# Optimization experiments

Hardware: AMD Instinct MI355X
Metric: run time of the kernel (lower is better)

## Reference

```python
import jax, jax.numpy as jnp
from jax import lax
import numpy as np

N = 400000   # active voxels
C = 32       # channels (in == out -> identity downsample)
G = 192      # voxel grid side
K = 27       # 3x3x3 kernel offsets
EPS = 1e-6


def _build_neighbor_map():
    """Rulebook for a 3^3 sparse conv: nbr[k, i] = input index of the voxel at
    coords[i] + offset[k], or -1 if that site is inactive."""
    rng = np.random.default_rng(0)
    keys = rng.choice(G ** 3, size=N, replace=False).astype(np.int64)
    xs = keys // (G * G)
    ys = (keys // G) % G
    zs = keys % G
    order = np.argsort(keys)
    sk = keys[order]
    nbr = np.full((K, N), -1, dtype=np.int32)
    k = 0
    for dx in (-1, 0, 1):
        for dy in (-1, 0, 1):
            for dz in (-1, 0, 1):
                nx, ny, nz = xs + dx, ys + dy, zs + dz
                inb = (nx >= 0) & (nx < G) & (ny >= 0) & (ny < G) & (nz >= 0) & (nz < G)
                nkey = nx * (G * G) + ny * G + nz
                pos = np.clip(np.searchsorted(sk, nkey), 0, N - 1)
                found = inb & (sk[pos] == nkey)
                nbr[k] = np.where(found, order[pos].astype(np.int32), -1)
                k += 1
    return nbr


def setup_inputs() -> dict:
    key = jax.random.key(0)
    k1, k2, k3 = jax.random.split(key, 3)
    scale = 1.0 / np.sqrt(K * C)
    x = jax.random.normal(k1, (N, C), dtype=jnp.float32)
    W1 = jax.random.normal(k2, (K, C, C), dtype=jnp.float32) * scale
    W2 = jax.random.normal(k3, (K, C, C), dtype=jnp.float32) * scale
    return {
        "x": x,
        "nbr": jnp.asarray(_build_neighbor_map()),
        "W1": W1,
        "g1": jnp.ones((C,), jnp.float32),
        "b1": jnp.zeros((C,), jnp.float32),
        "W2": W2,
        "g2": jnp.ones((C,), jnp.float32),
        "b2": jnp.zeros((C,), jnp.float32),
    }


def _sparse_conv(feats, W, nbr):
    # gather-GEMM-scatter over the 27 kernel offsets (stride=1: out sites == in sites)
    def body(acc, kw):
        idx, Wk = kw
        m = idx >= 0
        g = jnp.where(m[:, None], feats[jnp.maximum(idx, 0)], 0.0)  # [N, Cin]
        return acc + g @ Wk, None

    acc = jnp.zeros((feats.shape[0], W.shape[-1]), feats.dtype)
    acc, _ = lax.scan(body, acc, (nbr, W))
    return acc


def _layernorm(h, g, b):
    mu = jnp.mean(h, axis=-1, keepdims=True)
    var = jnp.mean(jnp.square(h - mu), axis=-1, keepdims=True)
    return (h - mu) * lax.rsqrt(var + EPS) * g + b


def reference(x, nbr, W1, g1, b1, W2, g2, b2):
    h = jax.nn.relu(_layernorm(_sparse_conv(x, W1, nbr), g1, b1))
    h = _layernorm(_sparse_conv(h, W2, nbr), g2, b2)
    # downsample is identity (in_channels == out_channels, stride == 1)
    return jax.nn.relu(h + x)
```

## Files before the change

### kernel.cpp

```cpp
#include <hip/hip_runtime.h>
#include <hip/hip_bf16.h>


#define NV 400000

typedef __bf16 bf16x8 __attribute__((ext_vector_type(8)));
typedef float  f32x4  __attribute__((ext_vector_type(4)));

union ABu { bf16x8 v; int4 i4; unsigned short us[8]; };

__device__ __forceinline__ unsigned short rb_f2bf(float f) {
    unsigned int u = __float_as_uint(f);
    return (unsigned short)((u + 0x7fffu + ((u >> 16) & 1u)) >> 16);
}

#define KIDX(kk) ((kk) + ((kk) >= 13 ? 1 : 0))

#define MFMA_BF16 __builtin_amdgcn_mfma_f32_16x16x32_bf16

__global__ __launch_bounds__(512) void xcvt_kernel(const float* __restrict__ xf,
                                                   unsigned short* __restrict__ xb)
{
    size_t i = ((size_t)blockIdx.x * 512 + threadIdx.x) * 8;
    float4 p0 = *(const float4*)(xf + i);
    float4 p1 = *(const float4*)(xf + i + 4);
    ABu a;
    a.us[0] = rb_f2bf(p0.x); a.us[1] = rb_f2bf(p0.y);
    a.us[2] = rb_f2bf(p0.z); a.us[3] = rb_f2bf(p0.w);
    a.us[4] = rb_f2bf(p1.x); a.us[5] = rb_f2bf(p1.y);
    a.us[6] = rb_f2bf(p1.z); a.us[7] = rb_f2bf(p1.w);
    *(int4*)(xb + i) = a.i4;
}

#define GATHER4(gbuf, jall)                                                   \
    do {                                                                      \
        _Pragma("unroll")                                                     \
        for (int _t = 0; _t < 4; ++_t) {                                      \
            int _j = __shfl((jall), _t * 16 + n);                             \
            gbuf[_t] = make_int4(0, 0, 0, 0);                                 \
            if (_j >= 0)                                                      \
                gbuf[_t] = *(const int4*)(gsrc + ((size_t)_j << 5) + qo);     \
        }                                                                     \
    } while (0)

#define CONSUME(kk, gbuf)                                                     \
    do {                                                                      \
        ABu _b0, _b1;                                                         \
        _b0.i4 = *(const int4*)(Bp + (kk) * 1024 + lane * 8);                 \
        _b1.i4 = *(const int4*)(Bp + (kk) * 1024 + 512 + lane * 8);           \
        _Pragma("unroll")                                                     \
        for (int _t = 0; _t < 4; ++_t) {                                      \
            ABu _a; _a.i4 = gbuf[_t];                                         \
            acc[_t][0] = MFMA_BF16(_a.v, _b0.v, acc[_t][0], 0, 0, 0);         \
            acc[_t][1] = MFMA_BF16(_a.v, _b1.v, acc[_t][1], 0, 0, 0);         \
        }                                                                     \
    } while (0)

template <bool WRITE_OUT>
__global__ __launch_bounds__(512, 4) void ResidualBlock_37452114821416_kernel(
    const float* __restrict__ xf,
    const int*   __restrict__ nbr,
    const float* __restrict__ Wf,
    const float* __restrict__ gf,
    const float* __restrict__ bfv,
    float*       __restrict__ outf,
    unsigned short* __restrict__ hbuf,
    const unsigned short* __restrict__ gsrc)
{
    __shared__ __align__(16) unsigned short Bp[26 * 1024];
    for (int e = threadIdx.x; e < 26 * 1024; e += 512) {
        int kk = e >> 10;
        int k  = KIDX(kk);
        int r  = e & 1023;
        int f  = r >> 9;
        int ll = (r >> 3) & 63;
        int j  = r & 7;
        int ci = ((ll >> 4) << 3) + j;
        int co = (ll & 15) + (f << 4);
        Bp[e] = rb_f2bf(Wf[k * 1024 + ci * 32 + co]);
    }

    const int  lane = threadIdx.x & 63;
    const int  wv   = threadIdx.x >> 6;
    const int  q    = lane >> 4, n = lane & 15;
    const int  i0   = blockIdx.x * 512 + wv * 64;
    const int  v64  = i0 + lane;
    const bool okv  = v64 < NV;
    const int  qo   = q * 8;

    ABu cb0, cb1;
    #pragma unroll
    for (int j = 0; j < 8; ++j) {
        int ci = (q << 3) + j;
        cb0.us[j] = rb_f2bf(Wf[13 * 1024 + ci * 32 + n]);
        cb1.us[j] = rb_f2bf(Wf[13 * 1024 + ci * 32 + n + 16]);
    }
    __syncthreads();

    f32x4 acc[4][2];
    #pragma unroll
    for (int t = 0; t < 4; ++t) {
        acc[t][0] = (f32x4){0.f, 0.f, 0.f, 0.f};
        acc[t][1] = (f32x4){0.f, 0.f, 0.f, 0.f};
    }

    int jA = okv ? __builtin_nontemporal_load(nbr + (size_t)KIDX(0) * NV + v64) : -1;
    int jB = okv ? __builtin_nontemporal_load(nbr + (size_t)KIDX(1) * NV + v64) : -1;

    int4 cgb[4];
    #pragma unroll
    for (int t = 0; t < 4; ++t) {
        int vt = i0 + t * 16 + n;
        cgb[t] = make_int4(0, 0, 0, 0);
        if (vt < NV) cgb[t] = *(const int4*)(gsrc + ((size_t)vt << 5) + qo);
    }

    int4 gA[4], gB[4];
    GATHER4(gA, jA);
    GATHER4(gB, jB);

    int jE = okv ? __builtin_nontemporal_load(nbr + (size_t)KIDX(2) * NV + v64) : -1;
    int jO = okv ? __builtin_nontemporal_load(nbr + (size_t)KIDX(3) * NV + v64) : -1;

    #pragma unroll
    for (int t = 0; t < 4; ++t) {
        ABu a; a.i4 = cgb[t];
        acc[t][0] = MFMA_BF16(a.v, cb0.v, acc[t][0], 0, 0, 0);
        acc[t][1] = MFMA_BF16(a.v, cb1.v, acc[t][1], 0, 0, 0);
    }

    #pragma unroll
    for (int p = 0; p < 13; ++p) {
        int jE2 = -1, jO2 = -1;
        if (2 * p + 4 < 26 && okv)
            jE2 = __builtin_nontemporal_load(nbr + (size_t)KIDX(2 * p + 4) * NV + v64);
        if (2 * p + 5 < 26 && okv)
            jO2 = __builtin_nontemporal_load(nbr + (size_t)KIDX(2 * p + 5) * NV + v64);

        CONSUME(2 * p, gA);
        if (2 * p + 2 < 26) GATHER4(gA, jE);

        CONSUME(2 * p + 1, gB);
        if (2 * p + 3 < 26) GATHER4(gB, jO);

        jE = jE2; jO = jO2;
    }

    const float gv0 = gf[n],  gv1 = gf[n + 16];
    const float bv0 = bfv[n], bv1 = bfv[n + 16];
    #pragma unroll
    for (int t = 0; t < 4; ++t) {
        #pragma unroll
        for (int r = 0; r < 4; ++r) {
            float x0 = acc[t][0][r], x1 = acc[t][1][r];
            float s  = x0 + x1;
            float ss = x0 * x0 + x1 * x1;
            #pragma unroll
            for (int mm = 1; mm <= 8; mm <<= 1) {
                s  += __shfl_xor(s, mm);
                ss += __shfl_xor(ss, mm);
            }
            float mu  = s * (1.f / 32.f);
            float var = ss * (1.f / 32.f) - mu * mu;
            float rs  = rsqrtf(var + 1e-6f);
            int vv = i0 + t * 16 + q * 4 + r;
            if (vv < NV) {
                float y0 = (x0 - mu) * rs * gv0 + bv0;
                float y1 = (x1 - mu) * rs * gv1 + bv1;
                if constexpr (WRITE_OUT) {
                    y0 += xf[(size_t)vv * 32 + n];
                    y1 += xf[(size_t)vv * 32 + n + 16];
                    outf[(size_t)vv * 32 + n]      = fmaxf(y0, 0.f);
                    outf[(size_t)vv * 32 + n + 16] = fmaxf(y1, 0.f);
                } else {
                    hbuf[(size_t)vv * 32 + n]      = rb_f2bf(fmaxf(y0, 0.f));
                    hbuf[(size_t)vv * 32 + n + 16] = rb_f2bf(fmaxf(y1, 0.f));
                }
            }
        }
    }
}

__global__ __launch_bounds__(512, 4) void pass1_f32_kernel(
    const float* __restrict__ xf, const int* __restrict__ nbr,
    const float* __restrict__ Wf, const float* __restrict__ gf,
    const float* __restrict__ bfv, unsigned short* __restrict__ hbuf)
{
    __shared__ __align__(16) unsigned short Bp[27 * 1024];
    for (int e = threadIdx.x; e < 27 * 1024; e += 512) {
        int k = e >> 10, r = e & 1023, f = r >> 9;
        int ll = (r >> 3) & 63, j = r & 7;
        int ci = ((ll >> 4) << 3) + j, co = (ll & 15) + (f << 4);
        Bp[e] = rb_f2bf(Wf[k * 1024 + ci * 32 + co]);
    }
    __syncthreads();
    const int lane = threadIdx.x & 63, wv = threadIdx.x >> 6;
    const int q = lane >> 4, n = lane & 15;
    const int i0 = blockIdx.x * 512 + wv * 64;
    f32x4 acc[4][2];
    #pragma unroll
    for (int t = 0; t < 4; ++t) { acc[t][0] = (f32x4){0,0,0,0}; acc[t][1] = (f32x4){0,0,0,0}; }
    for (int k = 0; k < 27; ++k) {
        ABu b0, b1;
        b0.i4 = *(const int4*)(Bp + k * 1024 + lane * 8);
        b1.i4 = *(const int4*)(Bp + k * 1024 + 512 + lane * 8);
        const int* nb = nbr + (size_t)k * NV;
        #pragma unroll
        for (int t = 0; t < 4; ++t) {
            int v = i0 + t * 16 + n;
            int jn = (v < NV) ? nb[v] : -1;
            if (__ballot(jn >= 0) == 0ull) continue;
            ABu a; a.i4 = make_int4(0, 0, 0, 0);
            if (jn >= 0) {
                const float* src = xf + (size_t)jn * 32 + q * 8;
                float4 p0 = *(const float4*)(src);
                float4 p1 = *(const float4*)(src + 4);
                a.us[0] = rb_f2bf(p0.x); a.us[1] = rb_f2bf(p0.y);
                a.us[2] = rb_f2bf(p0.z); a.us[3] = rb_f2bf(p0.w);
                a.us[4] = rb_f2bf(p1.x); a.us[5] = rb_f2bf(p1.y);
                a.us[6] = rb_f2bf(p1.z); a.us[7] = rb_f2bf(p1.w);
            }
            acc[t][0] = MFMA_BF16(a.v, b0.v, acc[t][0], 0, 0, 0);
            acc[t][1] = MFMA_BF16(a.v, b1.v, acc[t][1], 0, 0, 0);
        }
    }
    const float gv0 = gf[n], gv1 = gf[n + 16];
    const float bv0 = bfv[n], bv1 = bfv[n + 16];
    #pragma unroll
    for (int t = 0; t < 4; ++t) {
        #pragma unroll
        for (int r = 0; r < 4; ++r) {
            float x0 = acc[t][0][r], x1 = acc[t][1][r];
            float s = x0 + x1, ss = x0 * x0 + x1 * x1;
            #pragma unroll
            for (int mm = 1; mm <= 8; mm <<= 1) { s += __shfl_xor(s, mm); ss += __shfl_xor(ss, mm); }
            float mu = s * (1.f / 32.f);
            float var = ss * (1.f / 32.f) - mu * mu;
            float rs = rsqrtf(var + 1e-6f);
            int vv = i0 + t * 16 + q * 4 + r;
            if (vv < NV) {
                float y0 = (x0 - mu) * rs * gv0 + bv0;
                float y1 = (x1 - mu) * rs * gv1 + bv1;
                hbuf[(size_t)vv * 32 + n]      = rb_f2bf(fmaxf(y0, 0.f));
                hbuf[(size_t)vv * 32 + n + 16] = rb_f2bf(fmaxf(y1, 0.f));
            }
        }
    }
}

extern "C" void kernel_launch(void* const* d_in, const int* in_sizes, int n_in,
                              void* d_out, int out_size, void* d_ws, size_t ws_size,
                              hipStream_t stream)
{
    const float* x   = (const float*)d_in[0];
    const int*   nbr = (const int*)d_in[1];
    const float* W1  = (const float*)d_in[2];
    const float* g1  = (const float*)d_in[3];
    const float* b1  = (const float*)d_in[4];
    const float* W2  = (const float*)d_in[5];
    const float* g2  = (const float*)d_in[6];
    const float* b2  = (const float*)d_in[7];
    float* out = (float*)d_out;

    unsigned short* h  = (unsigned short*)d_ws;
    unsigned short* xb = h + (size_t)NV * 32;
    const bool have_xb = ws_size >= (size_t)NV * 32 * 2 * 2;

    const int nblk = (NV + 511) / 512;

    if (have_xb) {
        xcvt_kernel<<<3125, 512, 0, stream>>>(x, xb);
        ResidualBlock_37452114821416_kernel<false><<<nblk, 512, 0, stream>>>(
            x, nbr, W1, g1, b1, out, h, xb);
    } else {
        pass1_f32_kernel<<<nblk, 512, 0, stream>>>(x, nbr, W1, g1, b1, h);
    }
    ResidualBlock_37452114821416_kernel<true><<<nblk, 512, 0, stream>>>(
        x, nbr, W2, g2, b2, out, h, h);

    (void)in_sizes; (void)n_in; (void)out_size;
}
```

Before: 276.9 us.

## Halve voxels per wave and prefetch neighbor indices seven pairs deep

Each wave now handles 32 voxels instead of 64. Each neighbor-index load fetches two kernel offsets at once, using the two half-waves. Seven index pairs are issued up front, before the weights are staged into shared memory, and kept in a rotating register ring. Gathers are double-buffered by offset pair, and launch bounds are raised to 6 blocks per SM. The aim is to hide gather and index latency with more in-flight loads and more waves, at the cost of twice as many blocks each redoing the shared weight staging, and fewer MFMAs per B-fragment load.

```diff
diff --git a/kernel.cpp b/kernel.cpp
--- a/kernel.cpp
+++ b/kernel.cpp
@@ -32,32 +32,46 @@
     *(int4*)(xb + i) = a.i4;
 }
 
-#define GATHER4(gbuf, jall)                                                   \
+#define LOADIDX(P)                                                            \
+    (okv ? __builtin_nontemporal_load(                                        \
+               nbr + (size_t)KIDX(2 * (P)) * NV +                             \
+               (size_t)((KIDX(2 * (P) + 1) - KIDX(2 * (P))) * NVhi + vIdx))   \
+         : -1)
+
+#define GATHER_PAIR(S, JREG)                                                  \
     do {                                                                      \
         _Pragma("unroll")                                                     \
-        for (int _t = 0; _t < 4; ++_t) {                                      \
-            int _j = __shfl((jall), _t * 16 + n);                             \
-            gbuf[_t] = make_int4(0, 0, 0, 0);                                 \
-            if (_j >= 0)                                                      \
-                gbuf[_t] = *(const int4*)(gsrc + ((size_t)_j << 5) + qo);     \
+        for (int _h = 0; _h < 2; ++_h) {                                      \
+            _Pragma("unroll")                                                 \
+            for (int _t = 0; _t < 2; ++_t) {                                  \
+                int _j = __shfl((JREG), _h * 32 + _t * 16 + n);               \
+                g##S[_h][_t] = make_int4(0, 0, 0, 0);                         \
+                if (_j >= 0)                                                  \
+                    g##S[_h][_t] =                                            \
+                        *(const int4*)(gsrc + ((size_t)_j << 5) + qo);        \
+            }                                                                 \
         }                                                                     \
     } while (0)
 
-#define CONSUME(kk, gbuf)                                                     \
+#define CONSUME_PAIR(P, S)                                                    \
     do {                                                                      \
-        ABu _b0, _b1;                                                         \
-        _b0.i4 = *(const int4*)(Bp + (kk) * 1024 + lane * 8);                 \
-        _b1.i4 = *(const int4*)(Bp + (kk) * 1024 + 512 + lane * 8);           \
         _Pragma("unroll")                                                     \
-        for (int _t = 0; _t < 4; ++_t) {                                      \
-            ABu _a; _a.i4 = gbuf[_t];                                         \
-            acc[_t][0] = MFMA_BF16(_a.v, _b0.v, acc[_t][0], 0, 0, 0);         \
-            acc[_t][1] = MFMA_BF16(_a.v, _b1.v, acc[_t][1], 0, 0, 0);         \
+        for (int _h = 0; _h < 2; ++_h) {                                      \
+            const int _kk = 2 * (P) + _h;                                     \
+            ABu _b0, _b1;                                                     \
+            _b0.i4 = *(const int4*)(Bp + _kk * 1024 + lane * 8);              \
+            _b1.i4 = *(const int4*)(Bp + _kk * 1024 + 512 + lane * 8);        \
+            _Pragma("unroll")                                                 \
+            for (int _t = 0; _t < 2; ++_t) {                                  \
+                ABu _a; _a.i4 = g##S[_h][_t];                                 \
+                acc[_t][0] = MFMA_BF16(_a.v, _b0.v, acc[_t][0], 0, 0, 0);     \
+                acc[_t][1] = MFMA_BF16(_a.v, _b1.v, acc[_t][1], 0, 0, 0);     \
+            }                                                                 \
         }                                                                     \
     } while (0)
 
 template <bool WRITE_OUT>
-__global__ __launch_bounds__(512, 4) void ResidualBlock_37452114821416_kernel(
+__global__ __launch_bounds__(512, 6) void ResidualBlock_37452114821416_kernel(
     const float* __restrict__ xf,
     const int*   __restrict__ nbr,
     const float* __restrict__ Wf,
@@ -68,6 +82,36 @@
     const unsigned short* __restrict__ gsrc)
 {
     __shared__ __align__(16) unsigned short Bp[26 * 1024];
+
+    const int  lane = threadIdx.x & 63;
+    const int  wv   = threadIdx.x >> 6;
+    const int  q    = lane >> 4, n = lane & 15;
+    const int  i0w  = blockIdx.x * 256 + wv * 32;
+    const int  vIdx = i0w + (lane & 31);
+    const bool okv  = vIdx < NV;
+    const int  NVhi = (lane >= 32) ? NV : 0;
+    const int  qo   = q * 8;
+
+    int jn[7];
+    #pragma unroll
+    for (int p = 0; p < 7; ++p) jn[p] = LOADIDX(p);
+
+    int4 cg[2];
+    #pragma unroll
+    for (int t = 0; t < 2; ++t) {
+        int v = i0w + t * 16 + n;
+        cg[t] = make_int4(0, 0, 0, 0);
+        if (v < NV) cg[t] = *(const int4*)(gsrc + ((size_t)v << 5) + qo);
+    }
+
+    ABu cb0, cb1;
+    #pragma unroll
+    for (int j = 0; j < 8; ++j) {
+        int ci = (q << 3) + j;
+        cb0.us[j] = rb_f2bf(Wf[13 * 1024 + ci * 32 + n]);
+        cb1.us[j] = rb_f2bf(Wf[13 * 1024 + ci * 32 + n + 16]);
+    }
+
     for (int e = threadIdx.x; e < 26 * 1024; e += 512) {
         int kk = e >> 10;
         int k  = KIDX(kk);
@@ -79,77 +123,40 @@
         int co = (ll & 15) + (f << 4);
         Bp[e] = rb_f2bf(Wf[k * 1024 + ci * 32 + co]);
     }
-
-    const int  lane = threadIdx.x & 63;
-    const int  wv   = threadIdx.x >> 6;
-    const int  q    = lane >> 4, n = lane & 15;
-    const int  i0   = blockIdx.x * 512 + wv * 64;
-    const int  v64  = i0 + lane;
-    const bool okv  = v64 < NV;
-    const int  qo   = q * 8;
-
-    ABu cb0, cb1;
-    #pragma unroll
-    for (int j = 0; j < 8; ++j) {
-        int ci = (q << 3) + j;
-        cb0.us[j] = rb_f2bf(Wf[13 * 1024 + ci * 32 + n]);
-        cb1.us[j] = rb_f2bf(Wf[13 * 1024 + ci * 32 + n + 16]);
-    }
     __syncthreads();
 
-    f32x4 acc[4][2];
-    #pragma unroll
-    for (int t = 0; t < 4; ++t) {
+    f32x4 acc[2][2];
+    #pragma unroll
+    for (int t = 0; t < 2; ++t) {
         acc[t][0] = (f32x4){0.f, 0.f, 0.f, 0.f};
         acc[t][1] = (f32x4){0.f, 0.f, 0.f, 0.f};
     }
 
-    int jA = okv ? __builtin_nontemporal_load(nbr + (size_t)KIDX(0) * NV + v64) : -1;
-    int jB = okv ? __builtin_nontemporal_load(nbr + (size_t)KIDX(1) * NV + v64) : -1;
-
-    int4 cgb[4];
-    #pragma unroll
-    for (int t = 0; t < 4; ++t) {
-        int vt = i0 + t * 16 + n;
-        cgb[t] = make_int4(0, 0, 0, 0);
-        if (vt < NV) cgb[t] = *(const int4*)(gsrc + ((size_t)vt << 5) + qo);
-    }
-
-    int4 gA[4], gB[4];
-    GATHER4(gA, jA);
-    GATHER4(gB, jB);
-
-    int jE = okv ? __builtin_nontemporal_load(nbr + (size_t)KIDX(2) * NV + v64) : -1;
-    int jO = okv ? __builtin_nontemporal_load(nbr + (size_t)KIDX(3) * NV + v64) : -1;
-
-    #pragma unroll
-    for (int t = 0; t < 4; ++t) {
-        ABu a; a.i4 = cgb[t];
+    int4 gA[2][2], gB[2][2];
+    GATHER_PAIR(A, jn[0]);
+    #pragma unroll
+    for (int t = 0; t < 2; ++t) {
+        ABu a; a.i4 = cg[t];
         acc[t][0] = MFMA_BF16(a.v, cb0.v, acc[t][0], 0, 0, 0);
         acc[t][1] = MFMA_BF16(a.v, cb1.v, acc[t][1], 0, 0, 0);
     }
 
     #pragma unroll
     for (int p = 0; p < 13; ++p) {
-        int jE2 = -1, jO2 = -1;
-        if (2 * p + 4 < 26 && okv)
-            jE2 = __builtin_nontemporal_load(nbr + (size_t)KIDX(2 * p + 4) * NV + v64);
-        if (2 * p + 5 < 26 && okv)
-            jO2 = __builtin_nontemporal_load(nbr + (size_t)KIDX(2 * p + 5) * NV + v64);
-
-        CONSUME(2 * p, gA);
-        if (2 * p + 2 < 26) GATHER4(gA, jE);
-
-        CONSUME(2 * p + 1, gB);
-        if (2 * p + 3 < 26) GATHER4(gB, jO);
-
-        jE = jE2; jO = jO2;
+        if (p + 7 < 13) jn[p % 7] = LOADIDX(p + 7);
+        if ((p & 1) == 0) {
+            if (p + 1 < 13) GATHER_PAIR(B, jn[(p + 1) % 7]);
+            CONSUME_PAIR(p, A);
+        } else {
+            if (p + 1 < 13) GATHER_PAIR(A, jn[(p + 1) % 7]);
+            CONSUME_PAIR(p, B);
+        }
     }
 
     const float gv0 = gf[n],  gv1 = gf[n + 16];
     const float bv0 = bfv[n], bv1 = bfv[n + 16];
     #pragma unroll
-    for (int t = 0; t < 4; ++t) {
+    for (int t = 0; t < 2; ++t) {
         #pragma unroll
         for (int r = 0; r < 4; ++r) {
             float x0 = acc[t][0][r], x1 = acc[t][1][r];
@@ -163,7 +170,7 @@
             float mu  = s * (1.f / 32.f);
             float var = ss * (1.f / 32.f) - mu * mu;
             float rs  = rsqrtf(var + 1e-6f);
-            int vv = i0 + t * 16 + q * 4 + r;
+            int vv = i0w + t * 16 + q * 4 + r;
             if (vv < NV) {
                 float y0 = (x0 - mu) * rs * gv0 + bv0;
                 float y1 = (x1 - mu) * rs * gv1 + bv1;
@@ -266,14 +273,15 @@
     unsigned short* xb = h + (size_t)NV * 32;
     const bool have_xb = ws_size >= (size_t)NV * 32 * 2 * 2;
 
-    const int nblk = (NV + 511) / 512;
+    const int nblk = (NV + 255) / 256;
 
     if (have_xb) {
         xcvt_kernel<<<3125, 512, 0, stream>>>(x, xb);
         ResidualBlock_37452114821416_kernel<false><<<nblk, 512, 0, stream>>>(
             x, nbr, W1, g1, b1, out, h, xb);
     } else {
-        pass1_f32_kernel<<<nblk, 512, 0, stream>>>(x, nbr, W1, g1, b1, h);
+        pass1_f32_kernel<<<(NV + 511) / 512, 512, 0, stream>>>(
+            x, nbr, W1, g1, b1, h);
     }
     ResidualBlock_37452114821416_kernel<true><<<nblk, 512, 0, stream>>>(
         x, nbr, W2, g2, b2, out, h, h);
```

Result: slower. 290.2 us (+4.8%).

## Fuse convert and both conv passes into one cooperative persistent kernel

Applied to the files above, without the earlier changes.

Replaces the three launches (bf16 convert, conv1, conv2) with a single cooperative kernel of 512 persistent blocks that grid-stride over the 782 tiles. Stages are separated by grid-wide barriers, and each block rebuilds its LDS weight table per pass. The goal is to remove launch gaps and tail effects between kernels. In exchange it adds grid.sync cost and uneven tile distribution (782 tiles over 512 blocks gives some blocks two tiles). If the cooperative launch fails, the code falls back to separate kernels.

```diff
diff --git a/kernel.cpp b/kernel.cpp
--- a/kernel.cpp
+++ b/kernel.cpp
@@ -1,8 +1,13 @@
 #include <hip/hip_runtime.h>
 #include <hip/hip_bf16.h>
-
-
-#define NV 400000
+#include <hip/hip_cooperative_groups.h>
+
+namespace cg = cooperative_groups;
+
+
+#define NV   400000
+#define NT   782
+#define NBLK 512
 
 typedef __bf16 bf16x8 __attribute__((ext_vector_type(8)));
 typedef float  f32x4  __attribute__((ext_vector_type(4)));
@@ -18,18 +23,33 @@
 
 #define MFMA_BF16 __builtin_amdgcn_mfma_f32_16x16x32_bf16
 
-__global__ __launch_bounds__(512) void xcvt_kernel(const float* __restrict__ xf,
-                                                   unsigned short* __restrict__ xb)
-{
-    size_t i = ((size_t)blockIdx.x * 512 + threadIdx.x) * 8;
-    float4 p0 = *(const float4*)(xf + i);
-    float4 p1 = *(const float4*)(xf + i + 4);
-    ABu a;
-    a.us[0] = rb_f2bf(p0.x); a.us[1] = rb_f2bf(p0.y);
-    a.us[2] = rb_f2bf(p0.z); a.us[3] = rb_f2bf(p0.w);
-    a.us[4] = rb_f2bf(p1.x); a.us[5] = rb_f2bf(p1.y);
-    a.us[6] = rb_f2bf(p1.z); a.us[7] = rb_f2bf(p1.w);
-    *(int4*)(xb + i) = a.i4;
+
+__device__ __forceinline__ void fill_btable(unsigned short* Bp,
+                                            const float* __restrict__ Wf)
+{
+    for (int e = threadIdx.x; e < 26 * 1024; e += 512) {
+        int kk = e >> 10;
+        int k  = KIDX(kk);
+        int r  = e & 1023;
+        int f  = r >> 9;
+        int ll = (r >> 3) & 63;
+        int j  = r & 7;
+        int ci = ((ll >> 4) << 3) + j;
+        int co = (ll & 15) + (f << 4);
+        Bp[e] = rb_f2bf(Wf[k * 1024 + ci * 32 + co]);
+    }
+}
+
+__device__ __forceinline__ void load_center(ABu& cb0, ABu& cb1,
+                                            const float* __restrict__ Wf,
+                                            int q, int n)
+{
+    #pragma unroll
+    for (int j = 0; j < 8; ++j) {
+        int ci = (q << 3) + j;
+        cb0.us[j] = rb_f2bf(Wf[13 * 1024 + ci * 32 + n]);
+        cb1.us[j] = rb_f2bf(Wf[13 * 1024 + ci * 32 + n + 16]);
+    }
 }
 
 #define GATHER4(gbuf, jall)                                                   \
@@ -56,129 +76,192 @@
         }                                                                     \
     } while (0)
 
+#define NBLOAD(kk)                                                            \
+    (okv ? __builtin_nontemporal_load(nbr + (size_t)KIDX(kk) * NV + v64) : -1)
+
 template <bool WRITE_OUT>
-__global__ __launch_bounds__(512, 4) void ResidualBlock_37452114821416_kernel(
+__device__ __forceinline__ void conv_pass(
+    int start, int stride,
+    const unsigned short* Bp,
+    ABu cb0, ABu cb1,
     const float* __restrict__ xf,
     const int*   __restrict__ nbr,
-    const float* __restrict__ Wf,
     const float* __restrict__ gf,
     const float* __restrict__ bfv,
     float*       __restrict__ outf,
     unsigned short* __restrict__ hbuf,
     const unsigned short* __restrict__ gsrc)
 {
-    __shared__ __align__(16) unsigned short Bp[26 * 1024];
-    for (int e = threadIdx.x; e < 26 * 1024; e += 512) {
-        int kk = e >> 10;
-        int k  = KIDX(kk);
-        int r  = e & 1023;
-        int f  = r >> 9;
-        int ll = (r >> 3) & 63;
-        int j  = r & 7;
-        int ci = ((ll >> 4) << 3) + j;
-        int co = (ll & 15) + (f << 4);
-        Bp[e] = rb_f2bf(Wf[k * 1024 + ci * 32 + co]);
-    }
-
-    const int  lane = threadIdx.x & 63;
-    const int  wv   = threadIdx.x >> 6;
-    const int  q    = lane >> 4, n = lane & 15;
-    const int  i0   = blockIdx.x * 512 + wv * 64;
-    const int  v64  = i0 + lane;
-    const bool okv  = v64 < NV;
-    const int  qo   = q * 8;
-
-    ABu cb0, cb1;
-    #pragma unroll
-    for (int j = 0; j < 8; ++j) {
-        int ci = (q << 3) + j;
-        cb0.us[j] = rb_f2bf(Wf[13 * 1024 + ci * 32 + n]);
-        cb1.us[j] = rb_f2bf(Wf[13 * 1024 + ci * 32 + n + 16]);
-    }
-    __syncthreads();
-
-    f32x4 acc[4][2];
-    #pragma unroll
-    for (int t = 0; t < 4; ++t) {
-        acc[t][0] = (f32x4){0.f, 0.f, 0.f, 0.f};
-        acc[t][1] = (f32x4){0.f, 0.f, 0.f, 0.f};
-    }
-
-    int jA = okv ? __builtin_nontemporal_load(nbr + (size_t)KIDX(0) * NV + v64) : -1;
-    int jB = okv ? __builtin_nontemporal_load(nbr + (size_t)KIDX(1) * NV + v64) : -1;
-
-    int4 cgb[4];
-    #pragma unroll
-    for (int t = 0; t < 4; ++t) {
-        int vt = i0 + t * 16 + n;
-        cgb[t] = make_int4(0, 0, 0, 0);
-        if (vt < NV) cgb[t] = *(const int4*)(gsrc + ((size_t)vt << 5) + qo);
-    }
-
-    int4 gA[4], gB[4];
-    GATHER4(gA, jA);
-    GATHER4(gB, jB);
-
-    int jE = okv ? __builtin_nontemporal_load(nbr + (size_t)KIDX(2) * NV + v64) : -1;
-    int jO = okv ? __builtin_nontemporal_load(nbr + (size_t)KIDX(3) * NV + v64) : -1;
-
-    #pragma unroll
-    for (int t = 0; t < 4; ++t) {
-        ABu a; a.i4 = cgb[t];
-        acc[t][0] = MFMA_BF16(a.v, cb0.v, acc[t][0], 0, 0, 0);
-        acc[t][1] = MFMA_BF16(a.v, cb1.v, acc[t][1], 0, 0, 0);
-    }
-
-    #pragma unroll
-    for (int p = 0; p < 13; ++p) {
-        int jE2 = -1, jO2 = -1;
-        if (2 * p + 4 < 26 && okv)
-            jE2 = __builtin_nontemporal_load(nbr + (size_t)KIDX(2 * p + 4) * NV + v64);
-        if (2 * p + 5 < 26 && okv)
-            jO2 = __builtin_nontemporal_load(nbr + (size_t)KIDX(2 * p + 5) * NV + v64);
-
-        CONSUME(2 * p, gA);
-        if (2 * p + 2 < 26) GATHER4(gA, jE);
-
-        CONSUME(2 * p + 1, gB);
-        if (2 * p + 3 < 26) GATHER4(gB, jO);
-
-        jE = jE2; jO = jO2;
-    }
-
+    const int lane = threadIdx.x & 63;
+    const int wv   = threadIdx.x >> 6;
+    const int q    = lane >> 4, n = lane & 15;
+    const int qo   = q * 8;
     const float gv0 = gf[n],  gv1 = gf[n + 16];
     const float bv0 = bfv[n], bv1 = bfv[n + 16];
-    #pragma unroll
-    for (int t = 0; t < 4; ++t) {
-        #pragma unroll
-        for (int r = 0; r < 4; ++r) {
-            float x0 = acc[t][0][r], x1 = acc[t][1][r];
-            float s  = x0 + x1;
-            float ss = x0 * x0 + x1 * x1;
+
+    for (int tile = start; tile < NT; tile += stride) {
+        const int  i0  = tile * 512 + wv * 64;
+        const int  v64 = i0 + lane;
+        const bool okv = v64 < NV;
+
+        f32x4 acc[4][2];
+        #pragma unroll
+        for (int t = 0; t < 4; ++t) {
+            acc[t][0] = (f32x4){0.f, 0.f, 0.f, 0.f};
+            acc[t][1] = (f32x4){0.f, 0.f, 0.f, 0.f};
+        }
+
+        int jA = NBLOAD(0);
+        int jB = NBLOAD(1);
+
+        int4 cgb[4];
+        #pragma unroll
+        for (int t = 0; t < 4; ++t) {
+            int vt = i0 + t * 16 + n;
+            cgb[t] = make_int4(0, 0, 0, 0);
+            if (vt < NV) cgb[t] = *(const int4*)(gsrc + ((size_t)vt << 5) + qo);
+        }
+
+        int4 gA[4], gB[4];
+        GATHER4(gA, jA);
+        GATHER4(gB, jB);
+
+        int jE = NBLOAD(2);
+        int jO = NBLOAD(3);
+
+        #pragma unroll
+        for (int t = 0; t < 4; ++t) {
+            ABu a; a.i4 = cgb[t];
+            acc[t][0] = MFMA_BF16(a.v, cb0.v, acc[t][0], 0, 0, 0);
+            acc[t][1] = MFMA_BF16(a.v, cb1.v, acc[t][1], 0, 0, 0);
+        }
+
+        #pragma unroll
+        for (int p = 0; p < 13; ++p) {
+            int jE2 = -1, jO2 = -1;
+            if (2 * p + 4 < 26) jE2 = NBLOAD(2 * p + 4);
+            if (2 * p + 5 < 26) jO2 = NBLOAD(2 * p + 5);
+
+            CONSUME(2 * p, gA);
+            if (2 * p + 2 < 26) GATHER4(gA, jE);
+
+            CONSUME(2 * p + 1, gB);
+            if (2 * p + 3 < 26) GATHER4(gB, jO);
+
+            jE = jE2; jO = jO2;
+        }
+
+        #pragma unroll
+        for (int t = 0; t < 4; ++t) {
             #pragma unroll
-            for (int mm = 1; mm <= 8; mm <<= 1) {
-                s  += __shfl_xor(s, mm);
-                ss += __shfl_xor(ss, mm);
-            }
-            float mu  = s * (1.f / 32.f);
-            float var = ss * (1.f / 32.f) - mu * mu;
-            float rs  = rsqrtf(var + 1e-6f);
-            int vv = i0 + t * 16 + q * 4 + r;
-            if (vv < NV) {
-                float y0 = (x0 - mu) * rs * gv0 + bv0;
-                float y1 = (x1 - mu) * rs * gv1 + bv1;
-                if constexpr (WRITE_OUT) {
-                    y0 += xf[(size_t)vv * 32 + n];
-                    y1 += xf[(size_t)vv * 32 + n + 16];
-                    outf[(size_t)vv * 32 + n]      = fmaxf(y0, 0.f);
-                    outf[(size_t)vv * 32 + n + 16] = fmaxf(y1, 0.f);
-                } else {
-                    hbuf[(size_t)vv * 32 + n]      = rb_f2bf(fmaxf(y0, 0.f));
-                    hbuf[(size_t)vv * 32 + n + 16] = rb_f2bf(fmaxf(y1, 0.f));
+            for (int r = 0; r < 4; ++r) {
+                float x0 = acc[t][0][r], x1 = acc[t][1][r];
+                float s  = x0 + x1;
+                float ss = x0 * x0 + x1 * x1;
+                #pragma unroll
+                for (int mm = 1; mm <= 8; mm <<= 1) {
+                    s  += __shfl_xor(s, mm);
+                    ss += __shfl_xor(ss, mm);
+                }
+                float mu  = s * (1.f / 32.f);
+                float var = ss * (1.f / 32.f) - mu * mu;
+                float rs  = rsqrtf(var + 1e-6f);
+                int vv = i0 + t * 16 + q * 4 + r;
+                if (vv < NV) {
+                    float y0 = (x0 - mu) * rs * gv0 + bv0;
+                    float y1 = (x1 - mu) * rs * gv1 + bv1;
+                    if constexpr (WRITE_OUT) {
+                        y0 += xf[(size_t)vv * 32 + n];
+                        y1 += xf[(size_t)vv * 32 + n + 16];
+                        outf[(size_t)vv * 32 + n]      = fmaxf(y0, 0.f);
+                        outf[(size_t)vv * 32 + n + 16] = fmaxf(y1, 0.f);
+                    } else {
+                        hbuf[(size_t)vv * 32 + n]      = rb_f2bf(fmaxf(y0, 0.f));
+                        hbuf[(size_t)vv * 32 + n + 16] = rb_f2bf(fmaxf(y1, 0.f));
+                    }
                 }
             }
         }
     }
+}
+
+__global__ __launch_bounds__(512, 4) void ResidualBlock_37452114821416_kernel(
+    const float* __restrict__ xf,
+    const int*   __restrict__ nbr,
+    const float* __restrict__ W1f,
+    const float* __restrict__ g1f,
+    const float* __restrict__ b1f,
+    const float* __restrict__ W2f,
+    const float* __restrict__ g2f,
+    const float* __restrict__ b2f,
+    float*       __restrict__ outf,
+    unsigned short* __restrict__ hbuf,
+    unsigned short* __restrict__ xb)
+{
+    __shared__ __align__(16) unsigned short Bp[26 * 1024];
+    cg::grid_group grid = cg::this_grid();
+
+    const int q = (threadIdx.x & 63) >> 4;
+    const int n = threadIdx.x & 15;
+
+    for (size_t c = (size_t)blockIdx.x * 512 + threadIdx.x;
+         c < (size_t)NV * 32 / 8; c += (size_t)NBLK * 512) {
+        size_t i = c * 8;
+        float4 p0 = *(const float4*)(xf + i);
+        float4 p1 = *(const float4*)(xf + i + 4);
+        ABu a;
+        a.us[0] = rb_f2bf(p0.x); a.us[1] = rb_f2bf(p0.y);
+        a.us[2] = rb_f2bf(p0.z); a.us[3] = rb_f2bf(p0.w);
+        a.us[4] = rb_f2bf(p1.x); a.us[5] = rb_f2bf(p1.y);
+        a.us[6] = rb_f2bf(p1.z); a.us[7] = rb_f2bf(p1.w);
+        *(int4*)(xb + i) = a.i4;
+    }
+    grid.sync();
+
+    fill_btable(Bp, W1f);
+    ABu cb0, cb1;
+    load_center(cb0, cb1, W1f, q, n);
+    __syncthreads();
+    conv_pass<false>(blockIdx.x, NBLK, Bp, cb0, cb1,
+                     xf, nbr, g1f, b1f, outf, hbuf, xb);
+    grid.sync();
+
+    fill_btable(Bp, W2f);
+    load_center(cb0, cb1, W2f, q, n);
+    __syncthreads();
+    conv_pass<true>(blockIdx.x, NBLK, Bp, cb0, cb1,
+                    xf, nbr, g2f, b2f, outf, hbuf, hbuf);
+}
+
+
+__global__ __launch_bounds__(512) void xcvt_kernel(const float* __restrict__ xf,
+                                                   unsigned short* __restrict__ xb)
+{
+    size_t i = ((size_t)blockIdx.x * 512 + threadIdx.x) * 8;
+    float4 p0 = *(const float4*)(xf + i);
+    float4 p1 = *(const float4*)(xf + i + 4);
+    ABu a;
+    a.us[0] = rb_f2bf(p0.x); a.us[1] = rb_f2bf(p0.y);
+    a.us[2] = rb_f2bf(p0.z); a.us[3] = rb_f2bf(p0.w);
+    a.us[4] = rb_f2bf(p1.x); a.us[5] = rb_f2bf(p1.y);
+    a.us[6] = rb_f2bf(p1.z); a.us[7] = rb_f2bf(p1.w);
+    *(int4*)(xb + i) = a.i4;
+}
+
+template <bool WRITE_OUT>
+__global__ __launch_bounds__(512, 4) void pass_kernel(
+    const float* __restrict__ xf, const int* __restrict__ nbr,
+    const float* __restrict__ Wf, const float* __restrict__ gf,
+    const float* __restrict__ bfv, float* __restrict__ outf,
+    unsigned short* __restrict__ hbuf, const unsigned short* __restrict__ gsrc)
+{
+    __shared__ __align__(16) unsigned short Bp[26 * 1024];
+    fill_btable(Bp, Wf);
+    ABu cb0, cb1;
+    load_center(cb0, cb1, Wf, (threadIdx.x & 63) >> 4, threadIdx.x & 15);
+    __syncthreads();
+    conv_pass<WRITE_OUT>(blockIdx.x, gridDim.x, Bp, cb0, cb1,
+                         xf, nbr, gf, bfv, outf, hbuf, gsrc);
 }
 
 __global__ __launch_bounds__(512, 4) void pass1_f32_kernel(
@@ -266,17 +349,26 @@
     unsigned short* xb = h + (size_t)NV * 32;
     const bool have_xb = ws_size >= (size_t)NV * 32 * 2 * 2;
 
-    const int nblk = (NV + 511) / 512;
-
     if (have_xb) {
+        void* kargs[] = {
+            (void*)&x, (void*)&nbr, (void*)&W1, (void*)&g1, (void*)&b1,
+            (void*)&W2, (void*)&g2, (void*)&b2, (void*)&out, (void*)&h,
+            (void*)&xb
+        };
+        hipError_t ce = hipLaunchCooperativeKernel(
+            (const void*)ResidualBlock_37452114821416_kernel,
+            dim3(NBLK), dim3(512), kargs, 0, stream);
+        if (ce == hipSuccess) {
+            (void)in_sizes; (void)n_in; (void)out_size;
+            return;
+        }
+        (void)hipGetLastError();
         xcvt_kernel<<<3125, 512, 0, stream>>>(x, xb);
-        ResidualBlock_37452114821416_kernel<false><<<nblk, 512, 0, stream>>>(
-            x, nbr, W1, g1, b1, out, h, xb);
+        pass_kernel<false><<<NT, 512, 0, stream>>>(x, nbr, W1, g1, b1, out, h, xb);
     } else {
-        pass1_f32_kernel<<<nblk, 512, 0, stream>>>(x, nbr, W1, g1, b1, h);
-    }
-    ResidualBlock_37452114821416_kernel<true><<<nblk, 512, 0, stream>>>(
-        x, nbr, W2, g2, b2, out, h, h);
+        pass1_f32_kernel<<<NT, 512, 0, stream>>>(x, nbr, W1, g1, b1, h);
+    }
+    pass_kernel<true><<<NT, 512, 0, stream>>>(x, nbr, W2, g2, b2, out, h, h);
 
     (void)in_sizes; (void)n_in; (void)out_size;
 }
```

Measured after the change: 650.7 us. +135.0%, slower.

## Fuse fp32-to-bf16 conversion into first conv pass, drop separate xcvt kernel

Applied to the files above, without the earlier changes.

Removes the standalone kernel that converts x to bf16 and instead has the first sparse-conv pass gather fp32 rows directly, converting to bf16 in registers before the MFMAs, using the same double-buffered software-pipelined gather as the second pass. It also starts the first neighbor-index loads before the weight staging into shared memory. This saves one launch and one full read/write of x, but doubles gather bytes in pass 1 (fp32 rows) and adds register pressure from holding fp32 buffers.

```diff
diff --git a/kernel.cpp b/kernel.cpp
--- a/kernel.cpp
+++ b/kernel.cpp
@@ -3,6 +3,7 @@
 
 
 #define NV 400000
+#define NT 782
 
 typedef __bf16 bf16x8 __attribute__((ext_vector_type(8)));
 typedef float  f32x4  __attribute__((ext_vector_type(4)));
@@ -18,19 +19,163 @@
 
 #define MFMA_BF16 __builtin_amdgcn_mfma_f32_16x16x32_bf16
 
-__global__ __launch_bounds__(512) void xcvt_kernel(const float* __restrict__ xf,
-                                                   unsigned short* __restrict__ xb)
+
+#define GATHER4F(fb, jall)                                                    \
+    do {                                                                      \
+        _Pragma("unroll")                                                     \
+        for (int _t = 0; _t < 4; ++_t) {                                      \
+            int _j = __shfl((jall), _t * 16 + n);                             \
+            fb##0[_t] = make_float4(0.f, 0.f, 0.f, 0.f);                      \
+            fb##1[_t] = make_float4(0.f, 0.f, 0.f, 0.f);                      \
+            if (_j >= 0) {                                                    \
+                const float* _s = xf + ((size_t)_j << 5) + qo;                \
+                fb##0[_t] = *(const float4*)(_s);                             \
+                fb##1[_t] = *(const float4*)(_s + 4);                         \
+            }                                                                 \
+        }                                                                     \
+    } while (0)
+
+#define CONSUMEF(kk, fb)                                                      \
+    do {                                                                      \
+        ABu _b0, _b1;                                                         \
+        _b0.i4 = *(const int4*)(Bp + KIDX(kk) * 1024 + lane * 8);             \
+        _b1.i4 = *(const int4*)(Bp + KIDX(kk) * 1024 + 512 + lane * 8);       \
+        _Pragma("unroll")                                                     \
+        for (int _t = 0; _t < 4; ++_t) {                                      \
+            ABu _a;                                                           \
+            _a.us[0] = rb_f2bf(fb##0[_t].x); _a.us[1] = rb_f2bf(fb##0[_t].y); \
+            _a.us[2] = rb_f2bf(fb##0[_t].z); _a.us[3] = rb_f2bf(fb##0[_t].w); \
+            _a.us[4] = rb_f2bf(fb##1[_t].x); _a.us[5] = rb_f2bf(fb##1[_t].y); \
+            _a.us[6] = rb_f2bf(fb##1[_t].z); _a.us[7] = rb_f2bf(fb##1[_t].w); \
+            acc[_t][0] = MFMA_BF16(_a.v, _b0.v, acc[_t][0], 0, 0, 0);         \
+            acc[_t][1] = MFMA_BF16(_a.v, _b1.v, acc[_t][1], 0, 0, 0);         \
+        }                                                                     \
+    } while (0)
+
+__global__ __launch_bounds__(512, 4) void pass1_kernel(
+    const float* __restrict__ xf,
+    const int*   __restrict__ nbr,
+    const float* __restrict__ Wf,
+    const float* __restrict__ gf,
+    const float* __restrict__ bfv,
+    unsigned short* __restrict__ hbuf)
 {
-    size_t i = ((size_t)blockIdx.x * 512 + threadIdx.x) * 8;
-    float4 p0 = *(const float4*)(xf + i);
-    float4 p1 = *(const float4*)(xf + i + 4);
-    ABu a;
-    a.us[0] = rb_f2bf(p0.x); a.us[1] = rb_f2bf(p0.y);
-    a.us[2] = rb_f2bf(p0.z); a.us[3] = rb_f2bf(p0.w);
-    a.us[4] = rb_f2bf(p1.x); a.us[5] = rb_f2bf(p1.y);
-    a.us[6] = rb_f2bf(p1.z); a.us[7] = rb_f2bf(p1.w);
-    *(int4*)(xb + i) = a.i4;
+    __shared__ __align__(16) unsigned short Bp[27 * 1024];
+
+    const int  lane = threadIdx.x & 63;
+    const int  wv   = threadIdx.x >> 6;
+    const int  q    = lane >> 4, n = lane & 15;
+    const int  i0   = blockIdx.x * 512 + wv * 64;
+    const int  v64  = i0 + lane;
+    const bool okv  = v64 < NV;
+    const int  qo   = q * 8;
+
+    int jA = okv ? __builtin_nontemporal_load(nbr + (size_t)0 * NV + v64) : -1;
+    int jB = okv ? __builtin_nontemporal_load(nbr + (size_t)1 * NV + v64) : -1;
+
+    for (int e = threadIdx.x; e < 27 * 1024; e += 512) {
+        int k  = e >> 10;
+        int r  = e & 1023;
+        int f  = r >> 9;
+        int ll = (r >> 3) & 63;
+        int j  = r & 7;
+        int ci = ((ll >> 4) << 3) + j;
+        int co = (ll & 15) + (f << 4);
+        Bp[e] = rb_f2bf(Wf[k * 1024 + ci * 32 + co]);
+    }
+    __syncthreads();
+
+    f32x4 acc[4][2];
+    #pragma unroll
+    for (int t = 0; t < 4; ++t) {
+        acc[t][0] = (f32x4){0.f, 0.f, 0.f, 0.f};
+        acc[t][1] = (f32x4){0.f, 0.f, 0.f, 0.f};
+    }
+
+    {
+        ABu cb0, cb1;
+        cb0.i4 = *(const int4*)(Bp + 13 * 1024 + lane * 8);
+        cb1.i4 = *(const int4*)(Bp + 13 * 1024 + 512 + lane * 8);
+        #pragma unroll
+        for (int h2 = 0; h2 < 2; ++h2) {
+            float4 c0[2], c1[2];
+            #pragma unroll
+            for (int tt = 0; tt < 2; ++tt) {
+                int vt = i0 + (h2 * 2 + tt) * 16 + n;
+                c0[tt] = make_float4(0.f, 0.f, 0.f, 0.f);
+                c1[tt] = make_float4(0.f, 0.f, 0.f, 0.f);
+                if (vt < NV) {
+                    const float* s = xf + ((size_t)vt << 5) + qo;
+                    c0[tt] = *(const float4*)(s);
+                    c1[tt] = *(const float4*)(s + 4);
+                }
+            }
+            #pragma unroll
+            for (int tt = 0; tt < 2; ++tt) {
+                ABu a;
+                a.us[0] = rb_f2bf(c0[tt].x); a.us[1] = rb_f2bf(c0[tt].y);
+                a.us[2] = rb_f2bf(c0[tt].z); a.us[3] = rb_f2bf(c0[tt].w);
+                a.us[4] = rb_f2bf(c1[tt].x); a.us[5] = rb_f2bf(c1[tt].y);
+                a.us[6] = rb_f2bf(c1[tt].z); a.us[7] = rb_f2bf(c1[tt].w);
+                int t = h2 * 2 + tt;
+                acc[t][0] = MFMA_BF16(a.v, cb0.v, acc[t][0], 0, 0, 0);
+                acc[t][1] = MFMA_BF16(a.v, cb1.v, acc[t][1], 0, 0, 0);
+            }
+        }
+    }
+
+    float4 fA0[4], fA1[4], fB0[4], fB1[4];
+    GATHER4F(fA, jA);
+    GATHER4F(fB, jB);
+
+    int jE = okv ? __builtin_nontemporal_load(nbr + (size_t)KIDX(2) * NV + v64) : -1;
+    int jO = okv ? __builtin_nontemporal_load(nbr + (size_t)KIDX(3) * NV + v64) : -1;
+
+    #pragma unroll
+    for (int p = 0; p < 13; ++p) {
+        int jE2 = -1, jO2 = -1;
+        if (2 * p + 4 < 26 && okv)
+            jE2 = __builtin_nontemporal_load(nbr + (size_t)KIDX(2 * p + 4) * NV + v64);
+        if (2 * p + 5 < 26 && okv)
+            jO2 = __builtin_nontemporal_load(nbr + (size_t)KIDX(2 * p + 5) * NV + v64);
+
+        CONSUMEF(2 * p, fA);
+        if (2 * p + 2 < 26) GATHER4F(fA, jE);
+
+        CONSUMEF(2 * p + 1, fB);
+        if (2 * p + 3 < 26) GATHER4F(fB, jO);
+
+        jE = jE2; jO = jO2;
+    }
+
+    const float gv0 = gf[n],  gv1 = gf[n + 16];
+    const float bv0 = bfv[n], bv1 = bfv[n + 16];
+    #pragma unroll
+    for (int t = 0; t < 4; ++t) {
+        #pragma unroll
+        for (int r = 0; r < 4; ++r) {
+            float x0 = acc[t][0][r], x1 = acc[t][1][r];
+            float s  = x0 + x1;
+            float ss = x0 * x0 + x1 * x1;
+            #pragma unroll
+            for (int mm = 1; mm <= 8; mm <<= 1) {
+                s  += __shfl_xor(s, mm);
+                ss += __shfl_xor(ss, mm);
+            }
+            float mu  = s * (1.f / 32.f);
+            float var = ss * (1.f / 32.f) - mu * mu;
+            float rs  = rsqrtf(var + 1e-6f);
+            int vv = i0 + t * 16 + q * 4 + r;
+            if (vv < NV) {
+                float y0 = (x0 - mu) * rs * gv0 + bv0;
+                float y1 = (x1 - mu) * rs * gv1 + bv1;
+                hbuf[(size_t)vv * 32 + n]      = rb_f2bf(fmaxf(y0, 0.f));
+                hbuf[(size_t)vv * 32 + n + 16] = rb_f2bf(fmaxf(y1, 0.f));
+            }
+        }
+    }
 }
+
 
 #define GATHER4(gbuf, jall)                                                   \
     do {                                                                      \
@@ -56,15 +201,16 @@
         }                                                                     \
     } while (0)
 
-template <bool WRITE_OUT>
-__global__ __launch_bounds__(512, 4) void ResidualBlock_37452114821416_kernel(
+#define NBLOAD(kk)                                                            \
+    (okv ? __builtin_nontemporal_load(nbr + (size_t)KIDX(kk) * NV + v64) : -1)
+
+__global__ __launch_bounds__(512, 4) void pass2_kernel(
     const float* __restrict__ xf,
     const int*   __restrict__ nbr,
     const float* __restrict__ Wf,
     const float* __restrict__ gf,
     const float* __restrict__ bfv,
     float*       __restrict__ outf,
-    unsigned short* __restrict__ hbuf,
     const unsigned short* __restrict__ gsrc)
 {
     __shared__ __align__(16) unsigned short Bp[26 * 1024];
@@ -104,8 +250,8 @@
         acc[t][1] = (f32x4){0.f, 0.f, 0.f, 0.f};
     }
 
-    int jA = okv ? __builtin_nontemporal_load(nbr + (size_t)KIDX(0) * NV + v64) : -1;
-    int jB = okv ? __builtin_nontemporal_load(nbr + (size_t)KIDX(1) * NV + v64) : -1;
+    int jA = NBLOAD(0);
+    int jB = NBLOAD(1);
 
     int4 cgb[4];
     #pragma unroll
@@ -119,8 +265,8 @@
     GATHER4(gA, jA);
     GATHER4(gB, jB);
 
-    int jE = okv ? __builtin_nontemporal_load(nbr + (size_t)KIDX(2) * NV + v64) : -1;
-    int jO = okv ? __builtin_nontemporal_load(nbr + (size_t)KIDX(3) * NV + v64) : -1;
+    int jE = NBLOAD(2);
+    int jO = NBLOAD(3);
 
     #pragma unroll
     for (int t = 0; t < 4; ++t) {
@@ -132,10 +278,8 @@
     #pragma unroll
     for (int p = 0; p < 13; ++p) {
         int jE2 = -1, jO2 = -1;
-        if (2 * p + 4 < 26 && okv)
-            jE2 = __builtin_nontemporal_load(nbr + (size_t)KIDX(2 * p + 4) * NV + v64);
-        if (2 * p + 5 < 26 && okv)
-            jO2 = __builtin_nontemporal_load(nbr + (size_t)KIDX(2 * p + 5) * NV + v64);
+        if (2 * p + 4 < 26) jE2 = NBLOAD(2 * p + 4);
+        if (2 * p + 5 < 26) jO2 = NBLOAD(2 * p + 5);
 
         CONSUME(2 * p, gA);
         if (2 * p + 2 < 26) GATHER4(gA, jE);
@@ -165,84 +309,10 @@
             float rs  = rsqrtf(var + 1e-6f);
             int vv = i0 + t * 16 + q * 4 + r;
             if (vv < NV) {
-                float y0 = (x0 - mu) * rs * gv0 + bv0;
-                float y1 = (x1 - mu) * rs * gv1 + bv1;
-                if constexpr (WRITE_OUT) {
-                    y0 += xf[(size_t)vv * 32 + n];
-                    y1 += xf[(size_t)vv * 32 + n + 16];
-                    outf[(size_t)vv * 32 + n]      = fmaxf(y0, 0.f);
-                    outf[(size_t)vv * 32 + n + 16] = fmaxf(y1, 0.f);
-                } else {
-                    hbuf[(size_t)vv * 32 + n]      = rb_f2bf(fmaxf(y0, 0.f));
-                    hbuf[(size_t)vv * 32 + n + 16] = rb_f2bf(fmaxf(y1, 0.f));
-                }
-            }
-        }
-    }
-}
-
-__global__ __launch_bounds__(512, 4) void pass1_f32_kernel(
-    const float* __restrict__ xf, const int* __restrict__ nbr,
-    const float* __restrict__ Wf, const float* __restrict__ gf,
-    const float* __restrict__ bfv, unsigned short* __restrict__ hbuf)
-{
-    __shared__ __align__(16) unsigned short Bp[27 * 1024];
-    for (int e = threadIdx.x; e < 27 * 1024; e += 512) {
-        int k = e >> 10, r = e & 1023, f = r >> 9;
-        int ll = (r >> 3) & 63, j = r & 7;
-        int ci = ((ll >> 4) << 3) + j, co = (ll & 15) + (f << 4);
-        Bp[e] = rb_f2bf(Wf[k * 1024 + ci * 32 + co]);
-    }
-    __syncthreads();
-    const int lane = threadIdx.x & 63, wv = threadIdx.x >> 6;
-    const int q = lane >> 4, n = lane & 15;
-    const int i0 = blockIdx.x * 512 + wv * 64;
-    f32x4 acc[4][2];
-    #pragma unroll
-    for (int t = 0; t < 4; ++t) { acc[t][0] = (f32x4){0,0,0,0}; acc[t][1] = (f32x4){0,0,0,0}; }
-    for (int k = 0; k < 27; ++k) {
-        ABu b0, b1;
-        b0.i4 = *(const int4*)(Bp + k * 1024 + lane * 8);
-        b1.i4 = *(const int4*)(Bp + k * 1024 + 512 + lane * 8);
-        const int* nb = nbr + (size_t)k * NV;
-        #pragma unroll
-        for (int t = 0; t < 4; ++t) {
-            int v = i0 + t * 16 + n;
-            int jn = (v < NV) ? nb[v] : -1;
-            if (__ballot(jn >= 0) == 0ull) continue;
-            ABu a; a.i4 = make_int4(0, 0, 0, 0);
-            if (jn >= 0) {
-                const float* src = xf + (size_t)jn * 32 + q * 8;
-                float4 p0 = *(const float4*)(src);
-                float4 p1 = *(const float4*)(src + 4);
-                a.us[0] = rb_f2bf(p0.x); a.us[1] = rb_f2bf(p0.y);
-                a.us[2] = rb_f2bf(p0.z); a.us[3] = rb_f2bf(p0.w);
-                a.us[4] = rb_f2bf(p1.x); a.us[5] = rb_f2bf(p1.y);
-                a.us[6] = rb_f2bf(p1.z); a.us[7] = rb_f2bf(p1.w);
-            }
-            acc[t][0] = MFMA_BF16(a.v, b0.v, acc[t][0], 0, 0, 0);
-            acc[t][1] = MFMA_BF16(a.v, b1.v, acc[t][1], 0, 0, 0);
-        }
-    }
-    const float gv0 = gf[n], gv1 = gf[n + 16];
-    const float bv0 = bfv[n], bv1 = bfv[n + 16];
-    #pragma unroll
-    for (int t = 0; t < 4; ++t) {
-        #pragma unroll
-        for (int r = 0; r < 4; ++r) {
-            float x0 = acc[t][0][r], x1 = acc[t][1][r];
-            float s = x0 + x1, ss = x0 * x0 + x1 * x1;
-            #pragma unroll
-            for (int mm = 1; mm <= 8; mm <<= 1) { s += __shfl_xor(s, mm); ss += __shfl_xor(ss, mm); }
-            float mu = s * (1.f / 32.f);
-            float var = ss * (1.f / 32.f) - mu * mu;
-            float rs = rsqrtf(var + 1e-6f);
-            int vv = i0 + t * 16 + q * 4 + r;
-            if (vv < NV) {
-                float y0 = (x0 - mu) * rs * gv0 + bv0;
-                float y1 = (x1 - mu) * rs * gv1 + bv1;
-                hbuf[(size_t)vv * 32 + n]      = rb_f2bf(fmaxf(y0, 0.f));
-                hbuf[(size_t)vv * 32 + n + 16] = rb_f2bf(fmaxf(y1, 0.f));
+                float y0 = (x0 - mu) * rs * gv0 + bv0 + xf[(size_t)vv * 32 + n];
+                float y1 = (x1 - mu) * rs * gv1 + bv1 + xf[(size_t)vv * 32 + n + 16];
+                outf[(size_t)vv * 32 + n]      = fmaxf(y0, 0.f);
+                outf[(size_t)vv * 32 + n + 16] = fmaxf(y1, 0.f);
             }
         }
     }
@@ -262,21 +332,10 @@
     const float* b2  = (const float*)d_in[7];
     float* out = (float*)d_out;
 
-    unsigned short* h  = (unsigned short*)d_ws;
-    unsigned short* xb = h + (size_t)NV * 32;
-    const bool have_xb = ws_size >= (size_t)NV * 32 * 2 * 2;
-
-    const int nblk = (NV + 511) / 512;
-
-    if (have_xb) {
-        xcvt_kernel<<<3125, 512, 0, stream>>>(x, xb);
-        ResidualBlock_37452114821416_kernel<false><<<nblk, 512, 0, stream>>>(
-            x, nbr, W1, g1, b1, out, h, xb);
-    } else {
-        pass1_f32_kernel<<<nblk, 512, 0, stream>>>(x, nbr, W1, g1, b1, h);
-    }
-    ResidualBlock_37452114821416_kernel<true><<<nblk, 512, 0, stream>>>(
-        x, nbr, W2, g2, b2, out, h, h);
-
-    (void)in_sizes; (void)n_in; (void)out_size;
+    unsigned short* h = (unsigned short*)d_ws;
+
+    pass1_kernel<<<NT, 512, 0, stream>>>(x, nbr, W1, g1, b1, h);
+    pass2_kernel<<<NT, 512, 0, stream>>>(x, nbr, W2, g2, b2, out, h);
+
+    (void)in_sizes; (void)n_in; (void)out_size; (void)ws_size;
 }
```

New measurement: 330.7 us. 1.19x slower.
